# Kernel optimization log

Measured on AMD Instinct MI355X. Metric: run time of the kernel, lower is better.

Reference implementation:

```python
import jax, jax.numpy as jnp
import numpy as np

EPS = 1e-5

def _batchnorm(x, gamma, beta):
    # BatchNorm1d in training mode: stats over the point (N) dimension, biased var
    mean = x.mean(axis=0)
    var = ((x - mean) ** 2).mean(axis=0)
    return (x - mean) * jax.lax.rsqrt(var + EPS) * gamma + beta

def setup_inputs() -> dict:
    key = jax.random.key(0)
    ks = jax.random.split(key, 6)
    N, C_in, K, B = 262144, 3, 64, 16
    return {
        "feats": jax.random.normal(ks[0], (N, C_in), dtype=jnp.float32),
        "batch_idx": jax.random.randint(ks[1], (N,), 0, B, dtype=jnp.int32),
        "W1": jax.random.normal(ks[2], (128, C_in), dtype=jnp.float32) * 0.1,
        "gamma1": jnp.ones((128,), jnp.float32),
        "beta1": jnp.zeros((128,), jnp.float32),
        "W2": jax.random.normal(ks[3], (64, 256), dtype=jnp.float32) * 0.05,
        "gamma2": jnp.ones((64,), jnp.float32),
        "beta2": jnp.zeros((64,), jnp.float32),
        "W3": jax.random.normal(ks[4], (K, 64), dtype=jnp.float32) * 0.1,
        "b3": jnp.zeros((K,), jnp.float32),
        "num_batches": B,
    }

def reference(feats, batch_idx, W1, gamma1, beta1, W2, gamma2, beta2, W3, b3, num_batches):
    # conv1 (1x1 conv == linear, no bias) + bn1
    x = _batchnorm(feats @ W1.T, gamma1, beta1)          # [N,128]
    # per-batch global max pooling, broadcast back to points
    seg_max = jax.ops.segment_max(x, batch_idx, num_segments=num_batches)  # [B,128]
    x = jnp.concatenate([x, seg_max[batch_idx]], axis=1)  # [N,256]
    # conv2 + bn2 + relu
    x = jax.nn.relu(_batchnorm(x @ W2.T, gamma2, beta2))  # [N,64]
    # conv3 (with bias)
    return x @ W3.T + b3                                   # [N,k]
```

## Files before the change

kernel.cpp:

```cpp
#include <hip/hip_runtime.h>
#include <hip/hip_bf16.h>

#define EPS 1e-5f
#define NPTS 262144
#define NB 16
#define ACBLK 1024

typedef __attribute__((ext_vector_type(8))) short bf16x8;
typedef __attribute__((ext_vector_type(4))) float f32x4;

#define WS_E    0
#define WS_T    192
#define WS_W3   1216
#define WS_MAXG 3264
#define WS_PMOM 5312
#define WS_SCRM 6480
#define WS_PART 81232
#define WS_SMAX 114000

__device__ inline float decodeu(unsigned u){
  unsigned bits = (u & 0x80000000u) ? (u ^ 0x80000000u) : ~u;
  return __uint_as_float(bits);
}
__device__ inline unsigned f2bf(float f){
  unsigned u = __float_as_uint(f);
  return (u + 0x7FFFu + ((u>>16)&1u)) >> 16;
}
__device__ inline unsigned pack2bf(float lo, float hi){
  return (f2bf(hi)<<16) | (f2bf(lo) & 0xFFFFu);
}
__device__ inline unsigned ordu(float v){
  unsigned bits = __float_as_uint(v);
  return bits ^ (unsigned)(((int)bits>>31) | (int)0x80000000);
}

__global__ __launch_bounds__(256) void kAC(const float* __restrict__ feats,
                                           const int* __restrict__ bidx,
                                           const float* __restrict__ W1,
                                           const float* __restrict__ g1,
                                           float* __restrict__ wsf, int mode) {
  __shared__ unsigned lmax[NB*128];
  __shared__ __align__(16) float4 sfeat[256];
  __shared__ float hist[NB*4];
  __shared__ float red[4*9];
  int tid = threadIdx.x;
  for (int i=tid;i<NB*128;i+=256) lmax[i]=0u;
  if (tid < NB*4) hist[tid]=0.f;
  __syncthreads();
  int p = blockIdx.x*256 + tid;
  float f0=feats[3*p], f1=feats[3*p+1], f2=feats[3*p+2];
  int b = bidx[p];
  sfeat[tid] = make_float4(f0,f1,f2,__int_as_float(b));
  atomicAdd(&hist[b*4+0],f0);
  atomicAdd(&hist[b*4+1],f1);
  atomicAdd(&hist[b*4+2],f2);
  atomicAdd(&hist[b*4+3],1.0f);
  int lane = tid&63, wv = tid>>6;
  { float acc[9]={f0,f1,f2,f0*f0,f0*f1,f0*f2,f1*f1,f1*f2,f2*f2};
    #pragma unroll
    for (int k=0;k<9;k++){
      float v=acc[k];
      v+=__shfl_down(v,32); v+=__shfl_down(v,16); v+=__shfl_down(v,8);
      v+=__shfl_down(v,4);  v+=__shfl_down(v,2);  v+=__shfl_down(v,1);
      if (lane==0) red[wv*9+k]=v;
    }
  }
  __syncthreads();
  int c = (wv&1)*64 + lane;
  float sgn = (g1[c]>=0.f)?1.f:-1.f;
  float w0=W1[3*c]*sgn, w1=W1[3*c+1]*sgn, w2=W1[3*c+2]*sgn;
  const float4* sp = &sfeat[(wv>>1)*128];
  float m[16];
  #pragma unroll
  for (int q=0;q<16;q++) m[q] = -__builtin_inff();
  #pragma unroll 8
  for (int k=0;k<128;k++){
    float4 f = sp[k];
    float v = fmaf(f.z,w2,fmaf(f.y,w1,f.x*w0));
    int sbb = __builtin_amdgcn_readfirstlane(__float_as_int(f.w));
    switch (sbb){
      case 0:  m[0] = fmaxf(m[0], v); break;
      case 1:  m[1] = fmaxf(m[1], v); break;
      case 2:  m[2] = fmaxf(m[2], v); break;
      case 3:  m[3] = fmaxf(m[3], v); break;
      case 4:  m[4] = fmaxf(m[4], v); break;
      case 5:  m[5] = fmaxf(m[5], v); break;
      case 6:  m[6] = fmaxf(m[6], v); break;
      case 7:  m[7] = fmaxf(m[7], v); break;
      case 8:  m[8] = fmaxf(m[8], v); break;
      case 9:  m[9] = fmaxf(m[9], v); break;
      case 10: m[10] = fmaxf(m[10], v); break;
      case 11: m[11] = fmaxf(m[11], v); break;
      case 12: m[12] = fmaxf(m[12], v); break;
      case 13: m[13] = fmaxf(m[13], v); break;
      case 14: m[14] = fmaxf(m[14], v); break;
      default: m[15] = fmaxf(m[15], v); break;
    }
  }
  #pragma unroll
  for (int q=0;q<16;q++){
    if (m[q] > -__builtin_inff()) atomicMax(&lmax[q*128+c], ordu(m[q]));
  }
  __syncthreads();
  float* scrM = wsf + WS_SCRM + blockIdx.x*73;
  if (tid<9) scrM[tid]=red[tid]+red[9+tid]+red[18+tid]+red[27+tid];
  if (tid>=64 && tid<128) scrM[9+tid-64]=hist[tid-64];
  if (mode){
    unsigned* spo = (unsigned*)wsf + WS_SMAX + (size_t)blockIdx.x*2048;
    for (int i=tid;i<2048;i+=256) spo[i]=lmax[i];
  } else {
    unsigned* mg = (unsigned*)wsf + WS_MAXG;
    for (int i=tid;i<2048;i+=256){ unsigned v=lmax[i]; if(v) atomicMax(&mg[i],v); }
  }
}

__global__ __launch_bounds__(256) void kM(float* __restrict__ wsf){
  int g = blockIdx.x >> 3, ec = blockIdx.x & 7;
  int e = ec*256 + threadIdx.x;
  const unsigned* smax = (const unsigned*)wsf + WS_SMAX;
  unsigned m = 0;
  #pragma unroll 4
  for (int k=g*64;k<g*64+64;k++){ unsigned t=smax[(size_t)k*2048+e]; m = t>m?t:m; }
  ((unsigned*)wsf)[WS_PART + g*2048 + e] = m;
  if (ec==0 && threadIdx.x<73){
    float s=0; const float* sm0 = wsf + WS_SCRM;
    #pragma unroll 4
    for (int k=g*64;k<g*64+64;k++) s += sm0[k*73+threadIdx.x];
    wsf[WS_PMOM + g*73 + threadIdx.x] = s;
  }
}

__global__ __launch_bounds__(1024) void kB(float* __restrict__ wsf,
    const float* __restrict__ W1, const float* __restrict__ g1, const float* __restrict__ b1,
    const float* __restrict__ W2, const float* __restrict__ g2, const float* __restrict__ b2,
    const float* __restrict__ W3, int mode) {
  __shared__ __align__(16) float4 w2q[64*66];
  __shared__ __align__(16) float4 smbnq[NB*32];
  __shared__ __align__(16) float4 srhsq[4*32];
  __shared__ float s_w1[384];
  __shared__ float s_sc[128], s_sh[128], sE[3*64], sg[64], sT[NB*64];
  __shared__ float smom[80], s_s2[64], s_t2[64];
  int tid = threadIdx.x;
  float4 rw[4];
  #pragma unroll
  for (int t=0;t<4;t++) rw[t] = ((const float4*)W2)[tid + t*1024];
  float4 rw3 = ((const float4*)W3)[tid];
  if (tid<384) s_w1[tid]=W1[tid];
  #pragma unroll
  for (int t=0;t<4;t++){
    int q = tid + t*1024;
    w2q[(q&63)*66 + (q>>6)] = rw[t];
  }
  { unsigned* w3u = (unsigned*)wsf + WS_W3;
    w3u[2*tid]   = pack2bf(rw3.x, rw3.y);
    w3u[2*tid+1] = pack2bf(rw3.z, rw3.w);
  }
  if (mode){
    if (tid<73){ float s=0;
      #pragma unroll
      for (int g=0;g<16;g++) s += wsf[WS_PMOM+g*73+tid];
      smom[tid]=s; }
  } else {
    if (tid<73){ float s=0; const float* sm0=wsf+WS_SCRM;
      for (int k=0;k<ACBLK;k++) s += sm0[k*73+tid];
      smom[tid]=s; }
  }
  __syncthreads();
  const float invN = 1.0f/NPTS;
  if (tid < 128){
    int c=tid; float w0=s_w1[3*c],w1=s_w1[3*c+1],w2=s_w1[3*c+2];
    float mean = (w0*smom[0]+w1*smom[1]+w2*smom[2])*invN;
    float ex2 = (w0*w0*smom[3]+w1*w1*smom[6]+w2*w2*smom[8]
               + 2.f*(w0*w1*smom[4]+w0*w2*smom[5]+w1*w2*smom[7]))*invN;
    float var = ex2 - mean*mean;
    float sc = g1[c]*rsqrtf(var+EPS);
    s_sc[c]=sc; s_sh[c]=b1[c]-mean*sc;
  }
  __syncthreads();
  { const unsigned* part=(const unsigned*)wsf+WS_PART;
    const unsigned* mg=(const unsigned*)wsf+WS_MAXG;
    float* smbnf = (float*)smbnq;
    #pragma unroll
    for (int i=tid;i<NB*128;i+=1024){
      unsigned u;
      if (mode){ u=0;
        #pragma unroll
        for (int g=0;g<16;g++){ unsigned t=part[g*2048+i]; u = t>u?t:u; }
      } else u = mg[i];
      float M = decodeu(u);
      int ch=i&127;
      smbnf[i] = fabsf(s_sc[ch])*M + s_sh[ch];
    } }
  if (tid < 512){
    int which = tid>>7, j = tid&127;
    ((float*)srhsq)[tid] = (which<3) ? s_sc[j]*s_w1[3*j+which] : s_sh[j];
  }
  __syncthreads();
  { int c = tid&63, b = tid>>6;
    const float4* rq = &smbnq[b*32];
    float s=0;
    #pragma unroll 8
    for (int jj=0;jj<32;jj++){
      float4 a = w2q[(32+jj)*66 + c];
      float4 r = rq[jj];
      s = fmaf(a.x,r.x,fmaf(a.y,r.y,fmaf(a.z,r.z,fmaf(a.w,r.w,s))));
    }
    sT[b*64+c] = s;
    if (tid < 256){
      int which = tid>>6;
      float s2=0;
      #pragma unroll 8
      for (int jj=0;jj<32;jj++){
        float4 a = w2q[jj*66 + c];
        float4 r = srhsq[which*32+jj];
        s2 = fmaf(a.x,r.x,fmaf(a.y,r.y,fmaf(a.z,r.z,fmaf(a.w,r.w,s2))));
      }
      if (which<3) sE[which*64+c]=s2; else sg[c]=s2;
    }
  }
  __syncthreads();
  if (tid < 64){
    int c=tid;
    float e0=sE[c],e1=sE[64+c],e2=sE[128+c],gc=sg[c];
    float sumY = e0*smom[0]+e1*smom[1]+e2*smom[2];
    float sumYY = e0*e0*smom[3]+e1*e1*smom[6]+e2*e2*smom[8]
               + 2.f*(e0*e1*smom[4]+e0*e2*smom[5]+e1*e2*smom[7]);
    #pragma unroll
    for (int b=0;b<NB;b++){
      float nb = smom[9+b*4+3];
      float hb = gc + sT[b*64+c];
      float eS1b = e0*smom[9+b*4]+e1*smom[9+b*4+1]+e2*smom[9+b*4+2];
      sumY += nb*hb;
      sumYY += 2.f*hb*eS1b + nb*hb*hb;
    }
    float mean2 = sumY*invN;
    float var2 = sumYY*invN - mean2*mean2;
    float s2 = g2[c]*rsqrtf(var2+EPS);
    float t2 = b2[c]-mean2*s2;
    s_s2[c]=s2; s_t2[c]=t2;
    wsf[WS_E + c] = e0*s2; wsf[WS_E+64+c]=e1*s2; wsf[WS_E+128+c]=e2*s2;
  }
  __syncthreads();
  { int c=tid&63;
    if (tid < NB*64) wsf[WS_T + tid] = (sg[c]+sT[tid])*s_s2[c] + s_t2[c];
  }
}

__global__ __launch_bounds__(256) void kF(const float* __restrict__ feats,
                                          const int* __restrict__ bidx,
                                          const float* __restrict__ wsf,
                                          const float* __restrict__ b3,
                                          float* __restrict__ out) {
  __shared__ __align__(16) float Tl[NB*66];
  __shared__ __align__(16) unsigned zbuf[4*64*32];
  int tid = threadIdx.x;
  for (int i=tid;i<NB*64;i+=256) Tl[(i>>6)*66 + (i&63)] = wsf[WS_T + i];
  int lane = tid & 63, wv = tid >> 6;
  int col = lane & 15, kgrp = lane >> 4;
  const ushort* w3b = (const ushort*)((const unsigned*)wsf + WS_W3);
  bf16x8 bfr[4][2];
  #pragma unroll
  for (int n=0;n<4;n++)
    #pragma unroll
    for (int kk=0;kk<2;kk++)
      bfr[n][kk] = *(const bf16x8*)(w3b + (n*16+col)*64 + kk*32 + kgrp*8);
  float bias[4];
  #pragma unroll
  for (int n=0;n<4;n++) bias[n] = b3[n*16+col];
  __syncthreads();
  const float* Eg = wsf + WS_E;
  int p0 = (blockIdx.x*4 + wv)*64;
  int p = p0 + lane;
  float f0 = feats[3*p], f1 = feats[3*p+1], f2 = feats[3*p+2];
  int b = bidx[p];
  const float* tb = &Tl[b*66];
  unsigned rowbase = (unsigned)(wv*64+lane)*32;
  unsigned sw = (lane&7)<<2;
  #pragma unroll
  for (int j=0;j<8;j++){
    unsigned w[4];
    #pragma unroll
    for (int q=0;q<4;q++){
      int c = j*8 + q*2;
      float2 tp = *(const float2*)(tb + c);
      float y0 = fmaf(Eg[c],  f0, fmaf(Eg[64+c],  f1, fmaf(Eg[128+c],  f2, tp.x)));
      float y1 = fmaf(Eg[c+1],f0, fmaf(Eg[64+c+1],f1, fmaf(Eg[128+c+1],f2, tp.y)));
      w[q] = pack2bf(fmaxf(y0,0.f), fmaxf(y1,0.f));
    }
    uint4 ch; ch.x=w[0]; ch.y=w[1]; ch.z=w[2]; ch.w=w[3];
    *(uint4*)&zbuf[rowbase + (((unsigned)(j*4)) ^ sw)] = ch;
  }
  __syncthreads();
  bf16x8 af[4][2];
  #pragma unroll
  for (int m=0;m<4;m++){
    int row = m*16 + col;
    unsigned rb = (unsigned)(wv*64+row)*32;
    unsigned sw2 = (unsigned)(row&7)<<2;
    #pragma unroll
    for (int kk=0;kk<2;kk++){
      unsigned off = ((unsigned)(kk*16 + kgrp*4)) ^ sw2;
      af[m][kk] = *(const bf16x8*)&zbuf[rb + off];
    }
  }
  f32x4 acc[4][4];
  #pragma unroll
  for (int m=0;m<4;m++)
    #pragma unroll
    for (int n=0;n<4;n++)
      acc[m][n] = (f32x4){0.f,0.f,0.f,0.f};
  #pragma unroll
  for (int kk=0;kk<2;kk++)
    #pragma unroll
    for (int m=0;m<4;m++)
      #pragma unroll
      for (int n=0;n<4;n++)
        acc[m][n] = __builtin_amdgcn_mfma_f32_16x16x32_bf16(af[m][kk], bfr[n][kk], acc[m][n], 0,0,0);
  #pragma unroll
  for (int m=0;m<4;m++){
    int prow = p0 + m*16 + kgrp*4;
    #pragma unroll
    for (int n=0;n<4;n++){
      int cg = n*16+col;
      #pragma unroll
      for (int r=0;r<4;r++)
        out[(size_t)(prow+r)*64 + cg] = acc[m][n][r] + bias[n];
    }
  }
}

extern "C" void kernel_launch(void* const* d_in, const int* in_sizes, int n_in,
                              void* d_out, int out_size, void* d_ws, size_t ws_size,
                              hipStream_t stream) {
  const float* feats = (const float*)d_in[0];
  const int*   bidx  = (const int*)d_in[1];
  const float* W1 = (const float*)d_in[2];
  const float* g1 = (const float*)d_in[3];
  const float* b1 = (const float*)d_in[4];
  const float* W2 = (const float*)d_in[5];
  const float* g2 = (const float*)d_in[6];
  const float* b2 = (const float*)d_in[7];
  const float* W3 = (const float*)d_in[8];
  const float* b3 = (const float*)d_in[9];
  float* wsf = (float*)d_ws;
  float* out = (float*)d_out;
  size_t need = (size_t)(WS_SMAX + (size_t)ACBLK*2048)*4;
  int mode = (ws_size >= need) ? 1 : 0;
  if (!mode) (void)hipMemsetAsync((char*)d_ws + (size_t)WS_MAXG*4, 0, 2048*4, stream);
  kAC<<<ACBLK, 256, 0, stream>>>(feats, bidx, W1, g1, wsf, mode);
  if (mode) kM<<<128, 256, 0, stream>>>(wsf);
  kB<<<1, 1024, 0, stream>>>(wsf, W1,g1,b1, W2,g2,b2, W3, mode);
  kF<<<1024, 256, 0, stream>>>(feats, bidx, wsf, b3, out);
}
```

Measured before the change: 62.10 us.

## Stage MFMA output through LDS for coalesced float4 stores in kF

The final conv3 results are now written to a padded shared-memory buffer in two halves and then stored to global memory as row-contiguous float4 writes, instead of scattered per-lane scalar stores. The zbuf area is reused for this staging buffer and launch bounds request 4 blocks per CU. The aim is fewer, wider and better-coalesced global write transactions. In exchange it adds extra LDS traffic and several block-wide barriers, and the occupancy hint may constrain register allocation.

```diff
diff --git a/kernel.cpp b/kernel.cpp
--- a/kernel.cpp
+++ b/kernel.cpp
@@ -246,13 +246,15 @@
   }
 }
 
-__global__ __launch_bounds__(256) void kF(const float* __restrict__ feats,
-                                          const int* __restrict__ bidx,
-                                          const float* __restrict__ wsf,
-                                          const float* __restrict__ b3,
-                                          float* __restrict__ out) {
-  __shared__ __align__(16) float Tl[NB*66];
-  __shared__ __align__(16) unsigned zbuf[4*64*32];
+__global__ __launch_bounds__(256, 4) void kF(const float* __restrict__ feats,
+                                             const int* __restrict__ bidx,
+                                             const float* __restrict__ wsf,
+                                             const float* __restrict__ b3,
+                                             float* __restrict__ out) {
+  __shared__ __align__(16) unsigned char SB[36992];
+  unsigned* zbuf = (unsigned*)SB;
+  float* Tl = (float*)(SB + 32768);
+  float* fbuf = (float*)SB;
   int tid = threadIdx.x;
   for (int i=tid;i<NB*64;i+=256) Tl[(i>>6)*66 + (i&63)] = wsf[WS_T + i];
   int lane = tid & 63, wv = tid >> 6;
@@ -303,29 +305,42 @@
       af[m][kk] = *(const bf16x8*)&zbuf[rb + off];
     }
   }
-  f32x4 acc[4][4];
-  #pragma unroll
-  for (int m=0;m<4;m++)
-    #pragma unroll
-    for (int n=0;n<4;n++)
-      acc[m][n] = (f32x4){0.f,0.f,0.f,0.f};
-  #pragma unroll
-  for (int kk=0;kk<2;kk++)
-    #pragma unroll
-    for (int m=0;m<4;m++)
+  __syncthreads();
+  #pragma unroll
+  for (int half=0; half<2; half++){
+    f32x4 acc[2][4];
+    #pragma unroll
+    for (int mi=0;mi<2;mi++)
       #pragma unroll
       for (int n=0;n<4;n++)
-        acc[m][n] = __builtin_amdgcn_mfma_f32_16x16x32_bf16(af[m][kk], bfr[n][kk], acc[m][n], 0,0,0);
-  #pragma unroll
-  for (int m=0;m<4;m++){
-    int prow = p0 + m*16 + kgrp*4;
-    #pragma unroll
-    for (int n=0;n<4;n++){
-      int cg = n*16+col;
+        acc[mi][n] = (f32x4){0.f,0.f,0.f,0.f};
+    #pragma unroll
+    for (int kk=0;kk<2;kk++)
       #pragma unroll
-      for (int r=0;r<4;r++)
-        out[(size_t)(prow+r)*64 + cg] = acc[m][n][r] + bias[n];
-    }
+      for (int mi=0;mi<2;mi++)
+        #pragma unroll
+        for (int n=0;n<4;n++)
+          acc[mi][n] = __builtin_amdgcn_mfma_f32_16x16x32_bf16(af[half*2+mi][kk], bfr[n][kk], acc[mi][n], 0,0,0);
+    #pragma unroll
+    for (int mi=0;mi<2;mi++){
+      #pragma unroll
+      for (int n=0;n<4;n++){
+        #pragma unroll
+        for (int r=0;r<4;r++)
+          fbuf[wv*2176 + (mi*16 + kgrp*4 + r)*68 + n*16 + col] = acc[mi][n][r] + bias[n];
+      }
+    }
+    __syncthreads();
+    #pragma unroll
+    for (int it=0; it<8; it++){
+      int idx = it*256 + tid;
+      int gr = idx >> 4;
+      int c4 = (idx & 15) * 4;
+      float4 v = *(const float4*)&fbuf[(gr>>5)*2176 + (gr&31)*68 + c4];
+      int orow = blockIdx.x*256 + (gr>>5)*64 + half*32 + (gr&31);
+      *(float4*)&out[(size_t)orow*64 + c4] = v;
+    }
+    __syncthreads();
   }
 }
 
```

New measurement: 60.48 us. -2.6%, faster.
